# Kernel optimization log

Measured on AMD Instinct MI355X. Metric: run time of the kernel, lower is better.

Reference implementation:

```python
import jax, jax.numpy as jnp
import numpy as np

D_MODEL, D_K, C_DIM = 1024, 64, 64
B, S = 4, 4096


def setup_inputs() -> dict:
    key = jax.random.key(0)
    ks = jax.random.split(key, 10)
    sc = 1.0 / np.sqrt(D_MODEL)
    return {
        "X": jax.random.normal(ks[0], (B, S, D_MODEL), jnp.float32),
        "cultural_embedding": jax.random.normal(ks[1], (B, C_DIM), jnp.float32),
        "WQ": jax.random.normal(ks[2], (D_MODEL, D_K), jnp.float32) * sc,
        "bQ": jnp.zeros((D_K,), jnp.float32),
        "WK": jax.random.normal(ks[3], (D_MODEL, D_K), jnp.float32) * sc,
        "bK": jnp.zeros((D_K,), jnp.float32),
        "WV": jax.random.normal(ks[4], (D_MODEL, D_K), jnp.float32) * sc,
        "bV": jnp.zeros((D_K,), jnp.float32),
        "WC": jax.random.normal(ks[5], (C_DIM, D_K), jnp.float32) * (1.0 / np.sqrt(C_DIM)),
        "bC": jnp.zeros((D_K,), jnp.float32),
        "lam": jnp.float32(1.0),
    }


def reference(X, cultural_embedding, WQ, bQ, WK, bK, WV, bV, WC, bC, lam):
    # Projections: [B,S,d_k]
    Q = jnp.einsum('bsm,mk->bsk', X, WQ) + bQ
    K = jnp.einsum('bsm,mk->bsk', X, WK) + bK
    V = jnp.einsum('bsm,mk->bsk', X, WV) + bV
    # Cultural projection: [B,d_k]
    c_proj = cultural_embedding @ WC + bC
    # Base attention logits [B,S,S]
    base_logits = jnp.einsum('bqk,bsk->bqs', Q, K) / jnp.sqrt(jnp.float32(D_K))
    # Rank-1 cultural bias per query row, scalar lambda gate
    cultural_bias = lam * jnp.einsum('bsd,bd->bs', Q, c_proj)  # [B,S]
    combined = base_logits + cultural_bias[..., None]
    attn = jax.nn.softmax(combined, axis=-1)
    return jnp.einsum('bqs,bsk->bqk', attn, V)
```

## Files before the change

### kernel.cpp

```cpp
#include <hip/hip_runtime.h>

#define B_  4
#define S_  4096
#define DM  1024
#define DK  64
#define NSPLIT 8
#define KSPAN (S_ / NSPLIT)
#define QT  256

typedef _Float16 half8  __attribute__((ext_vector_type(8)));
typedef _Float16 half4v __attribute__((ext_vector_type(4)));
typedef __fp16   fp16x2 __attribute__((ext_vector_type(2)));
typedef float    floatx4 __attribute__((ext_vector_type(4)));

#define QSCALE 0.18033688011112042f
#define EXP2F(x) __builtin_amdgcn_exp2f(x)

__global__ __launch_bounds__(256) void wt_kernel(
    const float* __restrict__ WQ, const float* __restrict__ WK,
    const float* __restrict__ WV, _Float16* __restrict__ Wt)
{
    const int proj = blockIdx.y;
    const float* W = (proj == 0) ? WQ : (proj == 1) ? WK : WV;
    const int k0 = blockIdx.x * 64;
    const int t = threadIdx.x;
    __shared__ float T[64][68];

    #pragma unroll
    for (int p = 0; p < 4; p++) {
        int c = p * 256 + t;
        int k = c >> 4, n4 = (c & 15) * 4;
        float4 v = *(const float4*)(W + (size_t)(k0 + k) * DK + n4);
        T[k][n4 + 0] = v.x; T[k][n4 + 1] = v.y;
        T[k][n4 + 2] = v.z; T[k][n4 + 3] = v.w;
    }
    __syncthreads();

    const int n = t >> 2, kc = (t & 3) * 16;
    half8 h0, h1;
    #pragma unroll
    for (int j = 0; j < 8; j++) h0[j] = (_Float16)T[kc + j][n];
    #pragma unroll
    for (int j = 0; j < 8; j++) h1[j] = (_Float16)T[kc + 8 + j][n];
    _Float16* dst = Wt + ((size_t)proj * 64 + n) * DM + k0 + kc;
    *(half8*)(dst)     = h0;
    *(half8*)(dst + 8) = h1;
}

__global__ __launch_bounds__(256) void proj_mfma_kernel(
    const float* __restrict__ X, const _Float16* __restrict__ Wt,
    const float* __restrict__ bQ, const float* __restrict__ bK,
    const float* __restrict__ bV,
    _Float16* __restrict__ Qh, _Float16* __restrict__ Kh,
    _Float16* __restrict__ Vt)
{
    const int r0   = blockIdx.x * 64;
    const int t    = threadIdx.x;
    const int wave = t >> 6, lane = t & 63;
    const int quad = lane >> 4, l15 = lane & 15;

    __shared__ __align__(16) _Float16 Xs[64 * 72];
    __shared__ __align__(16) _Float16 Ws[3][64 * 72];

    floatx4 acc[3][4];
    #pragma unroll
    for (int p = 0; p < 3; p++)
        #pragma unroll
        for (int nt = 0; nt < 4; nt++)
            acc[p][nt] = (floatx4){0.f, 0.f, 0.f, 0.f};

    int xrow[4], xcol[4];
    #pragma unroll
    for (int p = 0; p < 4; p++) {
        int c = p * 256 + t;
        xrow[p] = c >> 4; xcol[p] = (c & 15) * 4;
    }
    int wrow[2], wcol[2];
    #pragma unroll
    for (int p = 0; p < 2; p++) {
        int c = p * 256 + t;
        wrow[p] = c >> 3; wcol[p] = (c & 7) * 8;
    }

    float4 xr[4]; half8 wr[3][2];
    #pragma unroll
    for (int p = 0; p < 4; p++)
        xr[p] = *(const float4*)(X + (size_t)(r0 + xrow[p]) * DM + xcol[p]);
    #pragma unroll
    for (int pr = 0; pr < 3; pr++)
        #pragma unroll
        for (int p = 0; p < 2; p++)
            wr[pr][p] = *(const half8*)(Wt + ((size_t)pr * 64 + wrow[p]) * DM + wcol[p]);

    for (int kt = 0; kt < DM / 64; kt++) {
        __syncthreads();
        #pragma unroll
        for (int p = 0; p < 4; p++) {
            half4v h;
            h[0] = (_Float16)xr[p].x; h[1] = (_Float16)xr[p].y;
            h[2] = (_Float16)xr[p].z; h[3] = (_Float16)xr[p].w;
            *(half4v*)&Xs[xrow[p] * 72 + xcol[p]] = h;
        }
        #pragma unroll
        for (int pr = 0; pr < 3; pr++)
            #pragma unroll
            for (int p = 0; p < 2; p++)
                *(half8*)&Ws[pr][wrow[p] * 72 + wcol[p]] = wr[pr][p];
        __syncthreads();

        if (kt + 1 < DM / 64) {
            const int kn = (kt + 1) * 64;
            #pragma unroll
            for (int p = 0; p < 4; p++)
                xr[p] = *(const float4*)(X + (size_t)(r0 + xrow[p]) * DM + kn + xcol[p]);
            #pragma unroll
            for (int pr = 0; pr < 3; pr++)
                #pragma unroll
                for (int p = 0; p < 2; p++)
                    wr[pr][p] = *(const half8*)(Wt + ((size_t)pr * 64 + wrow[p]) * DM + kn + wcol[p]);
        }

        half8 xa0 = *(half8*)&Xs[(wave * 16 + l15) * 72 + quad * 8];
        half8 xa1 = *(half8*)&Xs[(wave * 16 + l15) * 72 + 32 + quad * 8];
        #pragma unroll
        for (int pr = 0; pr < 3; pr++) {
            #pragma unroll
            for (int nt = 0; nt < 4; nt++) {
                half8 bf0 = *(half8*)&Ws[pr][(nt * 16 + l15) * 72 + quad * 8];
                half8 bf1 = *(half8*)&Ws[pr][(nt * 16 + l15) * 72 + 32 + quad * 8];
                floatx4 a = acc[pr][nt];
                a = __builtin_amdgcn_mfma_f32_16x16x32_f16(xa0, bf0, a, 0, 0, 0);
                a = __builtin_amdgcn_mfma_f32_16x16x32_f16(xa1, bf1, a, 0, 0, 0);
                acc[pr][nt] = a;
            }
        }
    }

    float bqv[4], bkv[4], bvv[4];
    #pragma unroll
    for (int nt = 0; nt < 4; nt++) {
        bqv[nt] = bQ[nt * 16 + l15];
        bkv[nt] = bK[nt * 16 + l15];
        bvv[nt] = bV[nt * 16 + l15];
    }

    const int orow = r0 + wave * 16 + quad * 4;
    const int bidx = r0 >> 12;
    const int s0   = (r0 & (S_ - 1)) + wave * 16 + quad * 4;
    #pragma unroll
    for (int nt = 0; nt < 4; nt++) {
        const int d = nt * 16 + l15;
        #pragma unroll
        for (int i = 0; i < 4; i++) {
            Qh[(size_t)(orow + i) * DK + d] =
                (_Float16)((acc[0][nt][i] + bqv[nt]) * QSCALE);
            Kh[(size_t)(orow + i) * DK + d] =
                (_Float16)(acc[1][nt][i] + bkv[nt]);
        }
        half4v hv;
        #pragma unroll
        for (int i = 0; i < 4; i++)
            hv[i] = (_Float16)(acc[2][nt][i] + bvv[nt]);
        *(half4v*)(Vt + (size_t)bidx * DK * S_ + (size_t)d * S_ + s0) = hv;
    }
}

__global__ __launch_bounds__(512, 4) void flash_mfma_kernel(
    const _Float16* __restrict__ Qh, const _Float16* __restrict__ Kh,
    const _Float16* __restrict__ Vt, _Float16* __restrict__ Oph,
    float* __restrict__ Lp)
{
    const int b     = blockIdx.y;
    const int q0    = blockIdx.x * QT;
    const int split = blockIdx.z;
    const int kbase = split * KSPAN;
    const int t     = threadIdx.x;
    const int wave  = t >> 6, lane = t & 63;
    const int quad  = lane >> 4, l15 = lane & 15;

    __shared__ __align__(16) _Float16 Ks[2][64 * 72];
    __shared__ __align__(16) _Float16 Vs[2][64 * 72];

    const _Float16* Qb = Qh + ((size_t)b * S_ + q0) * DK;
    const _Float16* Kb = Kh + ((size_t)b * S_ + kbase) * DK;
    const _Float16* Vb = Vt + (size_t)b * DK * S_ + kbase;

    half8 qf0[2], qf1[2];
    #pragma unroll
    for (int mt = 0; mt < 2; mt++) {
        const _Float16* qr = Qb + (size_t)(wave * 32 + mt * 16 + l15) * DK;
        qf0[mt] = *(const half8*)(qr + quad * 8);
        qf1[mt] = *(const half8*)(qr + 32 + quad * 8);
    }

    floatx4 acc[2][4];
    float rs[2];
    #pragma unroll
    for (int mt = 0; mt < 2; mt++) {
        #pragma unroll
        for (int nt = 0; nt < 4; nt++) acc[mt][nt] = (floatx4){0.f,0.f,0.f,0.f};
        rs[mt] = 0.f;
    }

    const int kr   = t >> 3, kcol = (t & 7) * 8;
    const int krP  = (kr & 32) | ((kr & 4) << 2) | ((kr & 24) >> 1) | (kr & 3);
    half8 kreg = *(const half8*)(Kb + (size_t)kr * DK + kcol);
    half8 vreg = *(const half8*)(Vb + (size_t)kr * S_ + kcol);
    *(half8*)&Ks[0][krP * 72 + kcol] = kreg;
    *(half8*)&Vs[0][kr  * 72 + kcol] = vreg;

    const int NT = KSPAN / 64;
    int cur = 0;
    for (int it = 0; it < NT; it++) {
        __syncthreads();

        if (it + 1 < NT) {
            const int kn = (it + 1) * 64;
            kreg = *(const half8*)(Kb + (size_t)(kn + kr) * DK + kcol);
            vreg = *(const half8*)(Vb + (size_t)kr * S_ + kn + kcol);
        }

        half8 pf0[2], pf1[2];
        #pragma unroll
        for (int nt = 0; nt < 4; nt++) {
            half8 kf0 = *(half8*)&Ks[cur][(nt * 16 + l15) * 72 + quad * 8];
            half8 kf1 = *(half8*)&Ks[cur][(nt * 16 + l15) * 72 + 32 + quad * 8];
            #pragma unroll
            for (int mt = 0; mt < 2; mt++) {
                floatx4 z = (floatx4){0.f, 0.f, 0.f, 0.f};
                z = __builtin_amdgcn_mfma_f32_16x16x32_f16(kf0, qf0[mt], z, 0, 0, 0);
                z = __builtin_amdgcn_mfma_f32_16x16x32_f16(kf1, qf1[mt], z, 0, 0, 0);
                float p0 = EXP2F(z[0]), p1 = EXP2F(z[1]);
                float p2 = EXP2F(z[2]), p3 = EXP2F(z[3]);
                rs[mt] += p0; rs[mt] += p1; rs[mt] += p2; rs[mt] += p3;
                fp16x2 ca = __builtin_amdgcn_cvt_pkrtz(p0, p1);
                fp16x2 cb = __builtin_amdgcn_cvt_pkrtz(p2, p3);
                if (nt < 2) {
                    pf0[mt][(nt & 1) * 4 + 0] = (_Float16)ca[0];
                    pf0[mt][(nt & 1) * 4 + 1] = (_Float16)ca[1];
                    pf0[mt][(nt & 1) * 4 + 2] = (_Float16)cb[0];
                    pf0[mt][(nt & 1) * 4 + 3] = (_Float16)cb[1];
                } else {
                    pf1[mt][(nt & 1) * 4 + 0] = (_Float16)ca[0];
                    pf1[mt][(nt & 1) * 4 + 1] = (_Float16)ca[1];
                    pf1[mt][(nt & 1) * 4 + 2] = (_Float16)cb[0];
                    pf1[mt][(nt & 1) * 4 + 3] = (_Float16)cb[1];
                }
            }
        }

        #pragma unroll
        for (int nt = 0; nt < 4; nt++) {
            half8 vf0 = *(half8*)&Vs[cur][(nt * 16 + l15) * 72 + quad * 8];
            half8 vf1 = *(half8*)&Vs[cur][(nt * 16 + l15) * 72 + 32 + quad * 8];
            #pragma unroll
            for (int mt = 0; mt < 2; mt++) {
                floatx4 a = acc[mt][nt];
                a = __builtin_amdgcn_mfma_f32_16x16x32_f16(vf0, pf0[mt], a, 0, 0, 0);
                a = __builtin_amdgcn_mfma_f32_16x16x32_f16(vf1, pf1[mt], a, 0, 0, 0);
                acc[mt][nt] = a;
            }
        }

        if (it + 1 < NT) {
            *(half8*)&Ks[cur ^ 1][krP * 72 + kcol] = kreg;
            *(half8*)&Vs[cur ^ 1][kr  * 72 + kcol] = vreg;
        }
        cur ^= 1;
    }

    const size_t prow = (size_t)split * B_ * S_ + (size_t)b * S_ + q0;
    #pragma unroll
    for (int mt = 0; mt < 2; mt++) {
        float r = rs[mt];
        r += __shfl_xor(r, 16, 64);
        r += __shfl_xor(r, 32, 64);
        const float inv = 1.0f / r;
        const size_t orow = prow + wave * 32 + mt * 16 + l15;
        #pragma unroll
        for (int nt = 0; nt < 4; nt++) {
            half4v hv;
            #pragma unroll
            for (int i = 0; i < 4; i++)
                hv[i] = (_Float16)(acc[mt][nt][i] * inv);
            *(half4v*)(Oph + orow * DK + nt * 16 + quad * 4) = hv;
        }
        if (quad == 0)
            Lp[orow] = r;
    }
}

__global__ __launch_bounds__(256) void combine_kernel(
    const _Float16* __restrict__ Oph, const float* __restrict__ Lp,
    float* __restrict__ O)
{
    const int r  = blockIdx.x * 16 + (threadIdx.x >> 4);
    const int d4 = (threadIdx.x & 15) * 4;
    const int NR = B_ * S_;

    float lw[NSPLIT], lsum = 0.f;
    #pragma unroll
    for (int s = 0; s < NSPLIT; s++) {
        lw[s] = Lp[(size_t)s * NR + r];
        lsum += lw[s];
    }
    const float inv = 1.0f / lsum;

    float o[4] = {0.f, 0.f, 0.f, 0.f};
    #pragma unroll
    for (int s = 0; s < NSPLIT; s++) {
        half4v h = *(const half4v*)(Oph + ((size_t)s * NR + r) * DK + d4);
        const float w = lw[s];
        #pragma unroll
        for (int j = 0; j < 4; j++) o[j] += w * (float)h[j];
    }
    float4 out;
    out.x = o[0] * inv; out.y = o[1] * inv;
    out.z = o[2] * inv; out.w = o[3] * inv;
    *(float4*)(O + (size_t)r * DK + d4) = out;
}

extern "C" void kernel_launch(void* const* d_in, const int* in_sizes, int n_in,
                              void* d_out, int out_size, void* d_ws, size_t ws_size,
                              hipStream_t stream)
{
    const float* X  = (const float*)d_in[0];
    const float* WQ = (const float*)d_in[2];
    const float* bQ = (const float*)d_in[3];
    const float* WK = (const float*)d_in[4];
    const float* bK = (const float*)d_in[5];
    const float* WV = (const float*)d_in[6];
    const float* bV = (const float*)d_in[7];

    char* ws = (char*)d_ws;
    _Float16* Qh  = (_Float16*)ws;  ws += (size_t)B_ * S_ * DK * 2;
    _Float16* Kh  = (_Float16*)ws;  ws += (size_t)B_ * S_ * DK * 2;
    _Float16* Vt  = (_Float16*)ws;  ws += (size_t)B_ * S_ * DK * 2;
    _Float16* Wt  = (_Float16*)ws;  ws += (size_t)3 * 64 * DM * 2;
    _Float16* Oph = (_Float16*)ws;  ws += (size_t)NSPLIT * B_ * S_ * DK * 2;
    float* Lp     = (float*)ws;

    wt_kernel<<<dim3(DM / 64, 3), 256, 0, stream>>>(WQ, WK, WV, Wt);

    proj_mfma_kernel<<<dim3((B_ * S_) / 64), 256, 0, stream>>>(
        X, Wt, bQ, bK, bV, Qh, Kh, Vt);

    flash_mfma_kernel<<<dim3(S_ / QT, B_, NSPLIT), 512, 0, stream>>>(
        Qh, Kh, Vt, Oph, Lp);

    combine_kernel<<<dim3((B_ * S_) / 16), 256, 0, stream>>>(
        Oph, Lp, (float*)d_out);
}
```

Before: 153.3 us.

## Split projection output columns across two blocks and raise MFMA wave priority

The projection kernel now launches two blocks per 64-row tile. Each block computes 96 of the 192 fused Q/K/V output columns, with the K columns divided between the halves. This doubles the grid from 256 to 512 blocks to improve occupancy and cuts per-thread accumulator registers, at the cost of reading and converting X twice. The flash kernel also wraps its two MFMA phases in s_setprio so waves issuing matrix work are favoured over waves doing loads.

Result: no change. 152.2 us, median of 2 (-0.7%).

```diff
diff --git a/kernel.cpp b/kernel.cpp
--- a/kernel.cpp
+++ b/kernel.cpp
@@ -55,19 +55,19 @@
     _Float16* __restrict__ Vt)
 {
     const int r0   = blockIdx.x * 64;
+    const int nh   = blockIdx.y;
     const int t    = threadIdx.x;
     const int wave = t >> 6, lane = t & 63;
     const int quad = lane >> 4, l15 = lane & 15;
 
     __shared__ __align__(16) _Float16 Xs[64 * 72];
-    __shared__ __align__(16) _Float16 Ws[3][64 * 72];
-
-    floatx4 acc[3][4];
-    #pragma unroll
-    for (int p = 0; p < 3; p++)
-        #pragma unroll
-        for (int nt = 0; nt < 4; nt++)
-            acc[p][nt] = (floatx4){0.f, 0.f, 0.f, 0.f};
+    __shared__ __align__(16) _Float16 Ws[96 * 72];
+
+    const _Float16* Wb = Wt + (size_t)(nh * 96) * DM;
+
+    floatx4 acc[6];
+    #pragma unroll
+    for (int j = 0; j < 6; j++) acc[j] = (floatx4){0.f, 0.f, 0.f, 0.f};
 
     int xrow[4], xcol[4];
     #pragma unroll
@@ -75,22 +75,20 @@
         int c = p * 256 + t;
         xrow[p] = c >> 4; xcol[p] = (c & 15) * 4;
     }
-    int wrow[2], wcol[2];
-    #pragma unroll
-    for (int p = 0; p < 2; p++) {
+    int wrow[3], wcol[3];
+    #pragma unroll
+    for (int p = 0; p < 3; p++) {
         int c = p * 256 + t;
         wrow[p] = c >> 3; wcol[p] = (c & 7) * 8;
     }
 
-    float4 xr[4]; half8 wr[3][2];
+    float4 xr[4]; half8 wr[3];
     #pragma unroll
     for (int p = 0; p < 4; p++)
         xr[p] = *(const float4*)(X + (size_t)(r0 + xrow[p]) * DM + xcol[p]);
     #pragma unroll
-    for (int pr = 0; pr < 3; pr++)
-        #pragma unroll
-        for (int p = 0; p < 2; p++)
-            wr[pr][p] = *(const half8*)(Wt + ((size_t)pr * 64 + wrow[p]) * DM + wcol[p]);
+    for (int p = 0; p < 3; p++)
+        wr[p] = *(const half8*)(Wb + (size_t)wrow[p] * DM + wcol[p]);
 
     for (int kt = 0; kt < DM / 64; kt++) {
         __syncthreads();
@@ -102,10 +100,8 @@
             *(half4v*)&Xs[xrow[p] * 72 + xcol[p]] = h;
         }
         #pragma unroll
-        for (int pr = 0; pr < 3; pr++)
-            #pragma unroll
-            for (int p = 0; p < 2; p++)
-                *(half8*)&Ws[pr][wrow[p] * 72 + wcol[p]] = wr[pr][p];
+        for (int p = 0; p < 3; p++)
+            *(half8*)&Ws[wrow[p] * 72 + wcol[p]] = wr[p];
         __syncthreads();
 
         if (kt + 1 < DM / 64) {
@@ -114,54 +110,66 @@
             for (int p = 0; p < 4; p++)
                 xr[p] = *(const float4*)(X + (size_t)(r0 + xrow[p]) * DM + kn + xcol[p]);
             #pragma unroll
-            for (int pr = 0; pr < 3; pr++)
-                #pragma unroll
-                for (int p = 0; p < 2; p++)
-                    wr[pr][p] = *(const half8*)(Wt + ((size_t)pr * 64 + wrow[p]) * DM + kn + wcol[p]);
+            for (int p = 0; p < 3; p++)
+                wr[p] = *(const half8*)(Wb + (size_t)wrow[p] * DM + kn + wcol[p]);
         }
 
         half8 xa0 = *(half8*)&Xs[(wave * 16 + l15) * 72 + quad * 8];
         half8 xa1 = *(half8*)&Xs[(wave * 16 + l15) * 72 + 32 + quad * 8];
         #pragma unroll
-        for (int pr = 0; pr < 3; pr++) {
-            #pragma unroll
-            for (int nt = 0; nt < 4; nt++) {
-                half8 bf0 = *(half8*)&Ws[pr][(nt * 16 + l15) * 72 + quad * 8];
-                half8 bf1 = *(half8*)&Ws[pr][(nt * 16 + l15) * 72 + 32 + quad * 8];
-                floatx4 a = acc[pr][nt];
-                a = __builtin_amdgcn_mfma_f32_16x16x32_f16(xa0, bf0, a, 0, 0, 0);
-                a = __builtin_amdgcn_mfma_f32_16x16x32_f16(xa1, bf1, a, 0, 0, 0);
-                acc[pr][nt] = a;
-            }
-        }
-    }
-
-    float bqv[4], bkv[4], bvv[4];
-    #pragma unroll
-    for (int nt = 0; nt < 4; nt++) {
-        bqv[nt] = bQ[nt * 16 + l15];
-        bkv[nt] = bK[nt * 16 + l15];
-        bvv[nt] = bV[nt * 16 + l15];
+        for (int j = 0; j < 6; j++) {
+            half8 bf0 = *(half8*)&Ws[(j * 16 + l15) * 72 + quad * 8];
+            half8 bf1 = *(half8*)&Ws[(j * 16 + l15) * 72 + 32 + quad * 8];
+            floatx4 a = acc[j];
+            a = __builtin_amdgcn_mfma_f32_16x16x32_f16(xa0, bf0, a, 0, 0, 0);
+            a = __builtin_amdgcn_mfma_f32_16x16x32_f16(xa1, bf1, a, 0, 0, 0);
+            acc[j] = a;
+        }
     }
 
     const int orow = r0 + wave * 16 + quad * 4;
     const int bidx = r0 >> 12;
     const int s0   = (r0 & (S_ - 1)) + wave * 16 + quad * 4;
-    #pragma unroll
-    for (int nt = 0; nt < 4; nt++) {
-        const int d = nt * 16 + l15;
-        #pragma unroll
-        for (int i = 0; i < 4; i++) {
-            Qh[(size_t)(orow + i) * DK + d] =
-                (_Float16)((acc[0][nt][i] + bqv[nt]) * QSCALE);
-            Kh[(size_t)(orow + i) * DK + d] =
-                (_Float16)(acc[1][nt][i] + bkv[nt]);
-        }
-        half4v hv;
-        #pragma unroll
-        for (int i = 0; i < 4; i++)
-            hv[i] = (_Float16)(acc[2][nt][i] + bvv[nt]);
-        *(half4v*)(Vt + (size_t)bidx * DK * S_ + (size_t)d * S_ + s0) = hv;
+
+    if (nh == 0) {
+        #pragma unroll
+        for (int j = 0; j < 4; j++) {
+            const int d = j * 16 + l15;
+            const float bq = bQ[d];
+            #pragma unroll
+            for (int i = 0; i < 4; i++)
+                Qh[(size_t)(orow + i) * DK + d] =
+                    (_Float16)((acc[j][i] + bq) * QSCALE);
+        }
+        #pragma unroll
+        for (int j = 4; j < 6; j++) {
+            const int d = (j - 4) * 16 + l15;
+            const float bk = bK[d];
+            #pragma unroll
+            for (int i = 0; i < 4; i++)
+                Kh[(size_t)(orow + i) * DK + d] =
+                    (_Float16)(acc[j][i] + bk);
+        }
+    } else {
+        #pragma unroll
+        for (int j = 0; j < 2; j++) {
+            const int d = (2 + j) * 16 + l15;
+            const float bk = bK[d];
+            #pragma unroll
+            for (int i = 0; i < 4; i++)
+                Kh[(size_t)(orow + i) * DK + d] =
+                    (_Float16)(acc[j][i] + bk);
+        }
+        #pragma unroll
+        for (int j = 2; j < 6; j++) {
+            const int d = (j - 2) * 16 + l15;
+            const float bv = bV[d];
+            half4v hv;
+            #pragma unroll
+            for (int i = 0; i < 4; i++)
+                hv[i] = (_Float16)(acc[j][i] + bv);
+            *(half4v*)(Vt + (size_t)bidx * DK * S_ + (size_t)d * S_ + s0) = hv;
+        }
     }
 }
 
@@ -221,6 +229,7 @@
         }
 
         half8 pf0[2], pf1[2];
+        __builtin_amdgcn_s_setprio(1);
         #pragma unroll
         for (int nt = 0; nt < 4; nt++) {
             half8 kf0 = *(half8*)&Ks[cur][(nt * 16 + l15) * 72 + quad * 8];
@@ -248,7 +257,9 @@
                 }
             }
         }
-
+        __builtin_amdgcn_s_setprio(0);
+
+        __builtin_amdgcn_s_setprio(1);
         #pragma unroll
         for (int nt = 0; nt < 4; nt++) {
             half8 vf0 = *(half8*)&Vs[cur][(nt * 16 + l15) * 72 + quad * 8];
@@ -261,6 +272,7 @@
                 acc[mt][nt] = a;
             }
         }
+        __builtin_amdgcn_s_setprio(0);
 
         if (it + 1 < NT) {
             *(half8*)&Ks[cur ^ 1][krP * 72 + kcol] = kreg;
@@ -342,7 +354,7 @@
 
     wt_kernel<<<dim3(DM / 64, 3), 256, 0, stream>>>(WQ, WK, WV, Wt);
 
-    proj_mfma_kernel<<<dim3((B_ * S_) / 64), 256, 0, stream>>>(
+    proj_mfma_kernel<<<dim3((B_ * S_) / 64, 2), 256, 0, stream>>>(
         X, Wt, bQ, bK, bV, Qh, Kh, Vt);
 
     flash_mfma_kernel<<<dim3(S_ / QT, B_, NSPLIT), 512, 0, stream>>>(
```
